# Kernel optimization log

Measured on AMD Instinct MI355X. Metric: run time of the kernel, lower is better.

The kernel has to match this reference:

```python
import jax, jax.numpy as jnp
import numpy as np

NS_STEPS = 10
NS_A, NS_B, NS_C = 3.4445, -4.7750, 2.0315  # standard quintic Newton-Schulz coefficients
EPS = 1e-7

def orthogonalize(w):
    """Newton-Schulz iteration producing a (near-)orthogonal matrix from w."""
    din, dout = w.shape
    transpose = din > dout  # iterate on the wide orientation so X @ X.T is small
    x = w.T if transpose else w
    x = x / (jnp.linalg.norm(x) + EPS)  # spectral norm <= frobenius norm -> contraction

    def body(x, _):
        a = x @ x.T                      # (m, m) Gram matrix
        bmat = NS_B * a + NS_C * (a @ a)
        x = NS_A * x + bmat @ x
        return x, None

    x, _ = jax.lax.scan(body, x, None, length=NS_STEPS)
    return x.T if transpose else x


def setup_inputs() -> dict:
    key = jax.random.key(0)
    k1, k2, k3 = jax.random.split(key, 3)
    B, DIN, DOUT = 16384, 2048, 2048
    x = jax.random.normal(k1, (B, DIN), dtype=jnp.float32)
    w = jax.random.normal(k2, (DIN, DOUT), dtype=jnp.float32)
    b = jax.random.normal(k3, (DOUT,), dtype=jnp.float32) * 0.02
    return {"x": x, "w": w, "b": b}


def reference(x, w, b):
    w_orth = orthogonalize(w)
    return x @ w_orth + b
```

## Files before the change

kernel.cpp:

```cpp
#include <hip/hip_runtime.h>
#include <stdint.h>

typedef unsigned short u16;
typedef _Float16 half_t;
typedef __attribute__((ext_vector_type(4))) float f32x4;
typedef __attribute__((ext_vector_type(8))) _Float16 f16x8;

#define NS_A 3.4445f
#define NS_B -4.7750f
#define NS_C 2.0315f

#define SX      64.0f
#define INV_SX  (1.0f / 64.0f)
#define INV_SA  (1.0f / 4096.0f)

typedef const __attribute__((address_space(1))) void* as1_cvp;
typedef __attribute__((address_space(3))) void* as3_vp;
#define GLOAD_LDS16(gp, lp) \
    __builtin_amdgcn_global_load_lds((as1_cvp)(const void*)(gp), (as3_vp)(void*)(lp), 16, 0, 0)

template <int N> __device__ __forceinline__ void vmwait() {
    if constexpr (N == 0)       asm volatile("s_waitcnt vmcnt(0)" ::: "memory");
    else if constexpr (N == 6)  asm volatile("s_waitcnt vmcnt(6)" ::: "memory");
    else static_assert(N == 0, "unsupported vmcnt");
}

template <int MODE>
__global__ __launch_bounds__(256, 2) void gemm_ns(
    const half_t* __restrict__ A, const half_t* __restrict__ B,
    const half_t* __restrict__ aux,
    void* __restrict__ outp, half_t* __restrict__ outpT,
    int M, int N, int K)
{
    __shared__ half_t As[3][64 * 64];
    __shared__ half_t Bs[3][128 * 64];
    const int tid  = threadIdx.x;
    const int wid  = tid >> 6;
    const int lane = tid & 63;
    const int wr = wid >> 1, wc = wid & 1;

    const int xcd = blockIdx.x & 7;
    const int ii  = blockIdx.x >> 3;
    const int brow = ((xcd & 1) * 16 + (ii >> 2)) * 64;
    const int bcol = ((xcd >> 1) * 4 + (ii & 3)) * 128;

    f32x4 acc[2][4] = {};

    const int r0   = tid >> 3;
    const int csrc = ((tid & 7) ^ ((tid >> 3) & 7)) * 8;
    const half_t* gA = A + (size_t)(brow + r0) * K + csrc;
    const half_t* gB = B + (size_t)(bcol + r0) * K + csrc;

    auto stage = [&](int slot, int kt) {
#pragma unroll
        for (int j = 0; j < 2; ++j)
            GLOAD_LDS16(gA + (size_t)(j * 32) * K + kt, &As[slot][(j * 256 + wid * 64) * 8]);
#pragma unroll
        for (int j = 0; j < 4; ++j)
            GLOAD_LDS16(gB + (size_t)(j * 32) * K + kt, &Bs[slot][(j * 256 + wid * 64) * 8]);
    };

    f16x8 af[2][2], bf[4][2];
    auto reads = [&](int slot) {
#pragma unroll
        for (int m = 0; m < 2; ++m) {
            const int row = wr * 32 + m * 16 + (lane & 15);
#pragma unroll
            for (int kk = 0; kk < 2; ++kk) {
                const int cc = (kk * 4 + (lane >> 4)) ^ (row & 7);
                af[m][kk] = *(const f16x8*)&As[slot][row * 64 + cc * 8];
            }
        }
#pragma unroll
        for (int n = 0; n < 4; ++n) {
            const int row = wc * 64 + n * 16 + (lane & 15);
#pragma unroll
            for (int kk = 0; kk < 2; ++kk) {
                const int cc = (kk * 4 + (lane >> 4)) ^ (row & 7);
                bf[n][kk] = *(const f16x8*)&Bs[slot][row * 64 + cc * 8];
            }
        }
    };
    auto mfma = [&]() {
        __builtin_amdgcn_s_setprio(1);
#pragma unroll
        for (int kk = 0; kk < 2; ++kk)
#pragma unroll
            for (int m = 0; m < 2; ++m)
#pragma unroll
                for (int n = 0; n < 4; ++n)
                    acc[m][n] = __builtin_amdgcn_mfma_f32_16x16x32_f16(af[m][kk], bf[n][kk], acc[m][n], 0, 0, 0);
        __builtin_amdgcn_s_setprio(0);
    };

    const int nsteps = K / 64;
    stage(0, 0);
    stage(1, 64);
    vmwait<6>();
    __builtin_amdgcn_s_barrier();

    int s = 0;
    for (; s < nsteps - 2; ++s) {
        reads(s % 3);
        stage((s + 2) % 3, (s + 2) * 64);
        vmwait<6>();
        __builtin_amdgcn_s_barrier();
        mfma();
        __builtin_amdgcn_s_barrier();
    }
    reads(s % 3);
    vmwait<0>();
    __builtin_amdgcn_s_barrier();
    mfma();
    __builtin_amdgcn_s_barrier();
    ++s;
    reads(s % 3);
    mfma();

#pragma unroll
    for (int m = 0; m < 2; ++m) {
#pragma unroll
        for (int n = 0; n < 4; ++n) {
            const int row0 = brow + wr * 32 + m * 16 + (lane >> 4) * 4;
            const int col  = bcol + wc * 64 + n * 16 + (lane & 15);
#pragma unroll
            for (int r = 0; r < 4; ++r) {
                const size_t idx = (size_t)(row0 + r) * N + col;
                const float v = acc[m][n][r];
                if (MODE == 0) {
                    ((half_t*)outp)[idx] = (half_t)v;
                } else if (MODE == 1) {
                    ((half_t*)outp)[idx] = (half_t)(NS_B * (float)aux[idx] + NS_C * v * INV_SA);
                } else {
                    const half_t o = (half_t)(NS_A * (float)aux[idx] + v * INV_SA);
                    if (outp)  ((half_t*)outp)[idx] = o;
                    if (outpT) outpT[(size_t)col * M + row0 + r] = o;
                }
            }
        }
    }
}

__global__ __launch_bounds__(512) void gemm_fin(
    const half_t* __restrict__ A, const half_t* __restrict__ B,
    const float* __restrict__ bias, float* __restrict__ out,
    int M, int N, int K)
{
    __shared__ half_t As[2][256 * 64];
    __shared__ half_t Bs[2][256 * 64];
    const int tid  = threadIdx.x;
    const int wid  = tid >> 6;
    const int lane = tid & 63;
    const int wm = wid >> 2;
    const int wn = wid & 3;

    int bid = blockIdx.x;
    const int cpx = gridDim.x >> 3;
    bid = (bid & 7) * cpx + (bid >> 3);
    const int nbx  = N >> 8;
    const int brow = (bid / nbx) << 8;
    const int bcol = (bid % nbx) << 8;

    f32x4 acc[8][4] = {};

    const int r0   = tid >> 3;
    const int csrc = ((tid & 7) ^ ((tid >> 3) & 7)) * 8;
    const half_t* gA = A + (size_t)(brow + r0) * K + csrc;
    const half_t* gB = B + (size_t)(bcol + r0) * K + csrc;

    auto stage = [&](int slot, int kt) {
#pragma unroll
        for (int j = 0; j < 4; ++j)
            GLOAD_LDS16(gA + (size_t)(j * 64) * K + kt, &As[slot][(j * 512 + wid * 64) * 8]);
#pragma unroll
        for (int j = 0; j < 4; ++j)
            GLOAD_LDS16(gB + (size_t)(j * 64) * K + kt, &Bs[slot][(j * 512 + wid * 64) * 8]);
    };
    auto compute = [&](int slot) {
        f16x8 af[8][2], bf[4][2];
#pragma unroll
        for (int fr = 0; fr < 8; ++fr) {
            const int row = wm * 128 + fr * 16 + (lane & 15);
#pragma unroll
            for (int kk = 0; kk < 2; ++kk) {
                const int cc = (kk * 4 + (lane >> 4)) ^ (row & 7);
                af[fr][kk] = *(const f16x8*)&As[slot][row * 64 + cc * 8];
            }
        }
#pragma unroll
        for (int fc = 0; fc < 4; ++fc) {
            const int row = wn * 64 + fc * 16 + (lane & 15);
#pragma unroll
            for (int kk = 0; kk < 2; ++kk) {
                const int cc = (kk * 4 + (lane >> 4)) ^ (row & 7);
                bf[fc][kk] = *(const f16x8*)&Bs[slot][row * 64 + cc * 8];
            }
        }
        __builtin_amdgcn_s_setprio(1);
#pragma unroll
        for (int kk = 0; kk < 2; ++kk)
#pragma unroll
            for (int fr = 0; fr < 8; ++fr)
#pragma unroll
                for (int fc = 0; fc < 4; ++fc)
                    acc[fr][fc] = __builtin_amdgcn_mfma_f32_16x16x32_f16(af[fr][kk], bf[fc][kk], acc[fr][fc], 0, 0, 0);
        __builtin_amdgcn_s_setprio(0);
    };

    const int nsteps = K >> 6;
    stage(0, 0);
    vmwait<0>();
    __builtin_amdgcn_s_barrier();

    for (int s = 0; s < nsteps; ++s) {
        const int slot = s & 1;
        if (s + 1 < nsteps) stage(slot ^ 1, (s + 1) * 64);
        compute(slot);
        if (s + 1 < nsteps) {
            vmwait<0>();
            __builtin_amdgcn_s_barrier();
        }
    }

#pragma unroll
    for (int fr = 0; fr < 8; ++fr) {
#pragma unroll
        for (int fc = 0; fc < 4; ++fc) {
            const int row0 = brow + wm * 128 + fr * 16 + (lane >> 4) * 4;
            const int col  = bcol + wn * 64 + fc * 16 + (lane & 15);
            const float bv = bias[col];
#pragma unroll
            for (int r = 0; r < 4; ++r)
                out[(size_t)(row0 + r) * N + col] = acc[fr][fc][r] * INV_SX + bv;
        }
    }
}

__global__ __launch_bounds__(256) void k_sumsq(const float* __restrict__ w,
                                               float* __restrict__ part, int n) {
    __shared__ float s[256];
    const int per  = n / 1024;
    const int base = blockIdx.x * per;
    float acc = 0.f;
    for (int i = threadIdx.x; i < per; i += 256) {
        float v = w[base + i];
        acc += v * v;
    }
    s[threadIdx.x] = acc;
    __syncthreads();
    for (int k = 128; k > 0; k >>= 1) {
        if (threadIdx.x < k) s[threadIdx.x] += s[threadIdx.x + k];
        __syncthreads();
    }
    if (threadIdx.x == 0) part[blockIdx.x] = s[0];
}

__global__ __launch_bounds__(256) void k_scalefin(const float* __restrict__ part,
                                                  float* __restrict__ scale) {
    __shared__ float s[256];
    float acc = 0.f;
    for (int i = threadIdx.x; i < 1024; i += 256) acc += part[i];
    s[threadIdx.x] = acc;
    __syncthreads();
    for (int k = 128; k > 0; k >>= 1) {
        if (threadIdx.x < k) s[threadIdx.x] += s[threadIdx.x + k];
        __syncthreads();
    }
    if (threadIdx.x == 0) scale[0] = SX / (sqrtf(s[0]) + 1e-7f);
}

__global__ __launch_bounds__(256) void k_scale_tr(const float* __restrict__ w,
                                                  const float* __restrict__ scale,
                                                  u16* __restrict__ o,
                                                  u16* __restrict__ oT, int n) {
    __shared__ u16 tile[64][65];
    const int bx = blockIdx.x * 64, by = blockIdx.y * 64;
    const int tx = threadIdx.x & 63, ty = threadIdx.x >> 6;
    const float sc = scale[0];
    for (int i = ty; i < 64; i += 4) {
        const half_t h = (half_t)(w[(size_t)(by + i) * n + bx + tx] * sc);
        const u16 u = __builtin_bit_cast(u16, h);
        o[(size_t)(by + i) * n + bx + tx] = u;
        tile[i][tx] = u;
    }
    __syncthreads();
    for (int i = ty; i < 64; i += 4)
        oT[(size_t)(bx + i) * n + by + tx] = tile[tx][i];
}

__global__ __launch_bounds__(256) void k_cast_f16(const float* __restrict__ w,
                                                  half_t* __restrict__ o, int n) {
    const int i = (blockIdx.x * 256 + threadIdx.x) * 4;
    if (i < n) {
        float4 v = *(const float4*)(w + i);
        o[i + 0] = (half_t)v.x;
        o[i + 1] = (half_t)v.y;
        o[i + 2] = (half_t)v.z;
        o[i + 3] = (half_t)v.w;
    }
}

__global__ __launch_bounds__(256) void k_transpose(const u16* __restrict__ in,
                                                   u16* __restrict__ out, int n) {
    __shared__ u16 tile[64][65];
    const int bx = blockIdx.x * 64, by = blockIdx.y * 64;
    const int tx = threadIdx.x & 63, ty = threadIdx.x >> 6;
    for (int i = ty; i < 64; i += 4) tile[i][tx] = in[(size_t)(by + i) * n + bx + tx];
    __syncthreads();
    for (int i = ty; i < 64; i += 4) out[(size_t)(bx + i) * n + by + tx] = tile[tx][i];
}

extern "C" void kernel_launch(void* const* d_in, const int* in_sizes, int n_in,
                              void* d_out, int out_size, void* d_ws, size_t ws_size,
                              hipStream_t stream) {
    const float* x = (const float*)d_in[0];
    const float* w = (const float*)d_in[1];
    const float* b = (const float*)d_in[2];
    float* out = (float*)d_out;

    const int D  = 2048;
    const int Bm = in_sizes[0] / D;
    const int WN = D * D;
    const int XN = Bm * D;

    const size_t matB = (size_t)WN * 2;
    const bool pingpong = ws_size >= 8192 + 6 * matB + (size_t)XN * 2;

    char* ws = (char*)d_ws;
    float* part  = (float*)ws;
    float* scale = part + 1024;
    half_t* xb0  = (half_t*)(ws + 8192);
    half_t* xb1  = xb0 + WN;
    half_t* xbTa = xb1 + WN;
    half_t* xbTb = pingpong ? (xbTa + WN) : xbTa;
    half_t* amat = xbTb + WN;
    half_t* bmat = amat + WN;
    half_t* xinb = bmat + WN;

    k_sumsq<<<1024, 256, 0, stream>>>(w, part, WN);
    k_scalefin<<<1, 256, 0, stream>>>(part, scale);
    const dim3 tgrid(D / 64, D / 64);
    k_scale_tr<<<tgrid, 256, 0, stream>>>(w, scale, (u16*)xb0, (u16*)xbTa, D);

    k_cast_f16<<<XN / 4 / 256, 256, 0, stream>>>(x, xinb, XN);

    const int ns_grid = (D / 64) * (D / 128);

    half_t* cur = xb0;
    half_t* nxt = xb1;
    half_t* Tr  = xbTa;
    half_t* Tw  = xbTb;
    for (int it = 0; it < 10; ++it) {
        gemm_ns<0><<<ns_grid, 256, 0, stream>>>(cur, cur, nullptr, amat, nullptr, D, D, D);
        gemm_ns<1><<<ns_grid, 256, 0, stream>>>(amat, amat, amat, bmat, nullptr, D, D, D);
        if (pingpong) {
            half_t* outp = (it == 9) ? nullptr : nxt;
            gemm_ns<2><<<ns_grid, 256, 0, stream>>>(bmat, Tr, cur, outp, Tw, D, D, D);
            half_t* tt = Tr; Tr = Tw; Tw = tt;
        } else {
            gemm_ns<2><<<ns_grid, 256, 0, stream>>>(bmat, Tr, cur, nxt, nullptr, D, D, D);
            k_transpose<<<tgrid, 256, 0, stream>>>((const u16*)nxt, (u16*)Tr, D);
        }
        half_t* t = cur; cur = nxt; nxt = t;
    }

    const int fin_grid = (Bm / 256) * (D / 256);
    gemm_fin<<<fin_grid, 512, 0, stream>>>(xinb, Tr, b, out, Bm, D, D);
}
```

Measured before the change: 943.4 us.

## Retile final GEMM to 128x256 with triple-buffered K=32 pipeline

The final x@W GEMM drops from 256x256 tiles with K=64 double buffering to 128x256 tiles with K=32 stages in a three-slot ring. Loads run two stages ahead with a partial vmcnt wait, and LDS reads for a stage are issued before its MFMAs. Shared memory per block shrinks and the grid doubles, which should improve occupancy and overlap memory with compute. In exchange there are more barriers per K step and less reuse per tile, since each block does less MFMA work per load.

```diff
diff --git a/kernel.cpp b/kernel.cpp
--- a/kernel.cpp
+++ b/kernel.cpp
@@ -21,6 +21,7 @@
 
 template <int N> __device__ __forceinline__ void vmwait() {
     if constexpr (N == 0)       asm volatile("s_waitcnt vmcnt(0)" ::: "memory");
+    else if constexpr (N == 3)  asm volatile("s_waitcnt vmcnt(3)" ::: "memory");
     else if constexpr (N == 6)  asm volatile("s_waitcnt vmcnt(6)" ::: "memory");
     else static_assert(N == 0, "unsupported vmcnt");
 }
@@ -146,8 +147,8 @@
     const float* __restrict__ bias, float* __restrict__ out,
     int M, int N, int K)
 {
-    __shared__ half_t As[2][256 * 64];
-    __shared__ half_t Bs[2][256 * 64];
+    __shared__ half_t As[3][128 * 32];
+    __shared__ half_t Bs[3][256 * 32];
     const int tid  = threadIdx.x;
     const int wid  = tid >> 6;
     const int lane = tid & 63;
@@ -158,75 +159,75 @@
     const int cpx = gridDim.x >> 3;
     bid = (bid & 7) * cpx + (bid >> 3);
     const int nbx  = N >> 8;
-    const int brow = (bid / nbx) << 8;
+    const int brow = (bid / nbx) << 7;
     const int bcol = (bid % nbx) << 8;
 
-    f32x4 acc[8][4] = {};
-
-    const int r0   = tid >> 3;
-    const int csrc = ((tid & 7) ^ ((tid >> 3) & 7)) * 8;
+    f32x4 acc[4][4] = {};
+
+    const int r0   = tid >> 2;
+    const int csrc = ((tid & 3) ^ ((tid >> 3) & 3)) * 8;
     const half_t* gA = A + (size_t)(brow + r0) * K + csrc;
     const half_t* gB = B + (size_t)(bcol + r0) * K + csrc;
 
     auto stage = [&](int slot, int kt) {
-#pragma unroll
-        for (int j = 0; j < 4; ++j)
-            GLOAD_LDS16(gA + (size_t)(j * 64) * K + kt, &As[slot][(j * 512 + wid * 64) * 8]);
-#pragma unroll
-        for (int j = 0; j < 4; ++j)
-            GLOAD_LDS16(gB + (size_t)(j * 64) * K + kt, &Bs[slot][(j * 512 + wid * 64) * 8]);
-    };
-    auto compute = [&](int slot) {
-        f16x8 af[8][2], bf[4][2];
-#pragma unroll
-        for (int fr = 0; fr < 8; ++fr) {
-            const int row = wm * 128 + fr * 16 + (lane & 15);
-#pragma unroll
-            for (int kk = 0; kk < 2; ++kk) {
-                const int cc = (kk * 4 + (lane >> 4)) ^ (row & 7);
-                af[fr][kk] = *(const f16x8*)&As[slot][row * 64 + cc * 8];
-            }
+        GLOAD_LDS16(gA + kt, &As[slot][(wid * 64) * 8]);
+#pragma unroll
+        for (int j = 0; j < 2; ++j)
+            GLOAD_LDS16(gB + (size_t)(j * 128) * K + kt, &Bs[slot][(j * 512 + wid * 64) * 8]);
+    };
+
+    f16x8 af[4], bf[4];
+    auto reads = [&](int slot) {
+#pragma unroll
+        for (int fr = 0; fr < 4; ++fr) {
+            const int row = wm * 64 + fr * 16 + (lane & 15);
+            af[fr] = *(const f16x8*)&As[slot][row * 32 + (((lane >> 4) ^ ((row >> 1) & 3)) * 8)];
         }
 #pragma unroll
         for (int fc = 0; fc < 4; ++fc) {
             const int row = wn * 64 + fc * 16 + (lane & 15);
-#pragma unroll
-            for (int kk = 0; kk < 2; ++kk) {
-                const int cc = (kk * 4 + (lane >> 4)) ^ (row & 7);
-                bf[fc][kk] = *(const f16x8*)&Bs[slot][row * 64 + cc * 8];
-            }
-        }
+            bf[fc] = *(const f16x8*)&Bs[slot][row * 32 + (((lane >> 4) ^ ((row >> 1) & 3)) * 8)];
+        }
+    };
+    auto mfma = [&]() {
         __builtin_amdgcn_s_setprio(1);
 #pragma unroll
-        for (int kk = 0; kk < 2; ++kk)
-#pragma unroll
-            for (int fr = 0; fr < 8; ++fr)
-#pragma unroll
-                for (int fc = 0; fc < 4; ++fc)
-                    acc[fr][fc] = __builtin_amdgcn_mfma_f32_16x16x32_f16(af[fr][kk], bf[fc][kk], acc[fr][fc], 0, 0, 0);
+        for (int fr = 0; fr < 4; ++fr)
+#pragma unroll
+            for (int fc = 0; fc < 4; ++fc)
+                acc[fr][fc] = __builtin_amdgcn_mfma_f32_16x16x32_f16(af[fr], bf[fc], acc[fr][fc], 0, 0, 0);
         __builtin_amdgcn_s_setprio(0);
     };
 
-    const int nsteps = K >> 6;
+    const int nsteps = K >> 5;
     stage(0, 0);
+    stage(1, 32);
+    vmwait<3>();
+    __builtin_amdgcn_s_barrier();
+
+    int s = 0;
+    for (; s < nsteps - 2; ++s) {
+        reads(s % 3);
+        stage((s + 2) % 3, (s + 2) * 32);
+        vmwait<3>();
+        __builtin_amdgcn_s_barrier();
+        mfma();
+        __builtin_amdgcn_s_barrier();
+    }
+    reads(s % 3);
     vmwait<0>();
     __builtin_amdgcn_s_barrier();
-
-    for (int s = 0; s < nsteps; ++s) {
-        const int slot = s & 1;
-        if (s + 1 < nsteps) stage(slot ^ 1, (s + 1) * 64);
-        compute(slot);
-        if (s + 1 < nsteps) {
-            vmwait<0>();
-            __builtin_amdgcn_s_barrier();
-        }
-    }
-
-#pragma unroll
-    for (int fr = 0; fr < 8; ++fr) {
+    mfma();
+    __builtin_amdgcn_s_barrier();
+    ++s;
+    reads(s % 3);
+    mfma();
+
+#pragma unroll
+    for (int fr = 0; fr < 4; ++fr) {
 #pragma unroll
         for (int fc = 0; fc < 4; ++fc) {
-            const int row0 = brow + wm * 128 + fr * 16 + (lane >> 4) * 4;
+            const int row0 = brow + wm * 64 + fr * 16 + (lane >> 4) * 4;
             const int col  = bcol + wn * 64 + fc * 16 + (lane & 15);
             const float bv = bias[col];
 #pragma unroll
@@ -364,6 +365,6 @@
         half_t* t = cur; cur = nxt; nxt = t;
     }
 
-    const int fin_grid = (Bm / 256) * (D / 256);
+    const int fin_grid = (Bm / 128) * (D / 256);
     gemm_fin<<<fin_grid, 512, 0, stream>>>(xinb, Tr, b, out, Bm, D, D);
 }
```

Measured after the change: 968.0 us. +2.6%, slower.
